# Kernel optimization log

Hardware: AMD Instinct MI355X
Metric: run time of the kernel (lower is better)

## Reference

```python
import jax, jax.numpy as jnp
import numpy as np

B = 131072
SD, AD, HID = 24, 8, 32
NH = SD + AD            # n_heads = 32
UNITS = HID * NH        # 1024


def _xavier(k, shape):
    fan_in, fan_out = shape[-2], shape[-1]
    lim = float(np.sqrt(6.0 / (fan_in + fan_out)))
    return jax.random.uniform(k, shape, jnp.float32, -lim, lim)


def setup_inputs() -> dict:
    key = jax.random.key(0)
    ks = jax.random.split(key, 8)
    return dict(
        state=jax.random.normal(ks[0], (B, SD), jnp.float32),
        action=jax.random.normal(ks[1], (B, AD), jnp.float32),
        # ripple layer 1: per-head Linear(NH -> HID), gate logits init 0 (init_prob=0.5)
        W1=_xavier(ks[2], (NH, NH, HID)), b1=jnp.zeros((NH, HID), jnp.float32), g1=jnp.zeros((NH,), jnp.float32),
        # ripple layer 2: per-head Linear(UNITS -> HID)
        W2=_xavier(ks[3], (NH, UNITS, HID)), b2=jnp.zeros((NH, HID), jnp.float32), g2=jnp.zeros((NH,), jnp.float32),
        # q_network
        Wq1=_xavier(ks[4], (UNITS, 256)), bq1=jnp.zeros((256,), jnp.float32),
        ln1_g=jnp.ones((256,), jnp.float32), ln1_b=jnp.zeros((256,), jnp.float32),
        Wq2=_xavier(ks[5], (256, 128)), bq2=jnp.zeros((128,), jnp.float32),
        ln2_g=jnp.ones((128,), jnp.float32), ln2_b=jnp.zeros((128,), jnp.float32),
        Wq3=_xavier(ks[6], (128, 1)), bq3=jnp.zeros((1,), jnp.float32),
    )


def _ripple(x, W, b, g):
    # x: [B, D]; W: [H, D, K]; per-head linear + tanh, scaled by per-head sigmoid gate
    h = jnp.tanh(jnp.einsum('bd,hdk->bhk', x, W) + b[None])  # [B, H, K]
    h = h * jax.nn.sigmoid(g)[None, :, None]
    return h.reshape(x.shape[0], -1)  # [B, H*K]


def _ln(x, g, b, eps=1e-5):
    mu = jnp.mean(x, -1, keepdims=True)
    var = jnp.mean((x - mu) ** 2, -1, keepdims=True)
    return (x - mu) * jax.lax.rsqrt(var + eps) * g + b


def reference(state, action, W1, b1, g1, W2, b2, g2,
              Wq1, bq1, ln1_g, ln1_b, Wq2, bq2, ln2_g, ln2_b, Wq3, bq3):
    sa = jnp.concatenate([state, action], axis=1)          # [B, SD+AD]
    x = _ripple(sa, W1, b1, g1)                            # [B, UNITS]
    x = _ripple(x, W2, b2, g2)                             # [B, UNITS]
    h = jax.nn.relu(_ln(x @ Wq1 + bq1, ln1_g, ln1_b))      # [B, 256] (dropout = eval identity)
    h = jax.nn.relu(_ln(h @ Wq2 + bq2, ln2_g, ln2_b))      # [B, 128]
    return h @ Wq3 + bq3                                   # [B, 1]
```

## Files before the change

kernel.cpp:

```cpp
#include <hip/hip_runtime.h>
#include <hip/hip_bf16.h>

typedef _Float16 f16x8 __attribute__((ext_vector_type(8)));
typedef float f32x4 __attribute__((ext_vector_type(4)));

__device__ __forceinline__ void async16(const _Float16* g, _Float16* l) {
  __builtin_amdgcn_global_load_lds(
      (const __attribute__((address_space(1))) unsigned int*)g,
      (__attribute__((address_space(3))) unsigned int*)l, 16, 0, 0);
}

__device__ __forceinline__ float tanh_fast(float x) {
  float e = __expf(2.0f * x);
  return 1.0f - 2.0f * __builtin_amdgcn_rcpf(e + 1.0f);
}
__device__ __forceinline__ float sigmoid_fast(float x) {
  return __builtin_amdgcn_rcpf(1.0f + __expf(-x));
}

__global__ __launch_bounds__(256) void transpose_all(
    const float* __restrict__ W1, const float* __restrict__ W2,
    const float* __restrict__ Wq1, const float* __restrict__ Wq2,
    _Float16* __restrict__ V1t, _Float16* __restrict__ V2t,
    _Float16* __restrict__ T1t, _Float16* __restrict__ T2t) {
  __shared__ float tile[32][33];
  int b = blockIdx.x;
  const float* in; _Float16* out; int R, C, rt, ct;
  if (b < 32) {
    in = W1 + b * 1024; out = V1t + b * 1024; R = 32; C = 32; rt = 0; ct = 0;
  } else if (b < 32 + 1024) {
    int i = b - 32; int z = i >> 5;
    in = W2 + (size_t)z * 32768; out = V2t + (size_t)z * 32768;
    R = 1024; C = 32; rt = i & 31; ct = 0;
  } else if (b < 32 + 1024 + 256) {
    int i = b - 1056; in = Wq1; out = T1t; R = 1024; C = 256; rt = i >> 3; ct = i & 7;
  } else {
    int i = b - 1312; in = Wq2; out = T2t; R = 256; C = 128; rt = i >> 2; ct = i & 3;
  }
  int r0 = rt * 32, c0 = ct * 32;
  int t = threadIdx.x;
  int cc = t & 31, rr8 = t >> 5;
#pragma unroll
  for (int p = 0; p < 4; ++p) {
    int r = rr8 + p * 8;
    tile[cc][r] = in[(size_t)(r0 + r) * C + c0 + cc];
  }
  __syncthreads();
  int rr = t & 31, cc8 = t >> 5;
#pragma unroll
  for (int p = 0; p < 4; ++p) {
    int c = cc8 + p * 8;
    out[(size_t)(c0 + c) * R + r0 + rr] = (_Float16)tile[c][rr];
  }
}

__global__ __launch_bounds__(256) void k1_ripple1(
    const float* __restrict__ state, const float* __restrict__ action,
    const _Float16* __restrict__ v1t, const float* __restrict__ b1,
    const float* __restrict__ g1, _Float16* __restrict__ x1, int gro) {
  __shared__ __align__(16) _Float16 As[128 * 40];
  int bn = blockIdx.x, bm = blockIdx.y;
  int t = threadIdx.x, w = t >> 6, l = t & 63, q = l >> 4, l15 = l & 15;
  int n0 = bn * 128, m0 = bm * 128;

  {
    int r = t >> 1, half = t & 1;
    size_t grow = (size_t)(gro + m0 + r);
    float v[16];
    if (half == 0) {
      const float4* sp = (const float4*)(state + grow * 24);
      ((float4*)v)[0] = sp[0]; ((float4*)v)[1] = sp[1];
      ((float4*)v)[2] = sp[2]; ((float4*)v)[3] = sp[3];
    } else {
      const float4* sp = (const float4*)(state + grow * 24 + 16);
      ((float4*)v)[0] = sp[0]; ((float4*)v)[1] = sp[1];
      const float4* ap = (const float4*)(action + grow * 8);
      ((float4*)v)[2] = ap[0]; ((float4*)v)[3] = ap[1];
    }
    f16x8 h0, h1;
#pragma unroll
    for (int j = 0; j < 8; ++j) { h0[j] = (_Float16)v[j]; h1[j] = (_Float16)v[8 + j]; }
    *(f16x8*)&As[r * 40 + half * 16] = h0;
    *(f16x8*)&As[r * 40 + half * 16 + 8] = h1;
  }
  __syncthreads();

  int wr = w >> 1, wc = w & 1;
  f16x8 af[4], bf[4];
#pragma unroll
  for (int mi = 0; mi < 4; ++mi)
    af[mi] = *(const f16x8*)&As[(wr * 64 + mi * 16 + l15) * 40 + q * 8];
#pragma unroll
  for (int ni = 0; ni < 4; ++ni)
    bf[ni] = *(const f16x8*)(v1t + (size_t)(n0 + wc * 64 + ni * 16 + l15) * 32 + q * 8);

  f32x4 acc[4][4] = {};
#pragma unroll
  for (int mi = 0; mi < 4; ++mi)
#pragma unroll
    for (int ni = 0; ni < 4; ++ni)
      acc[mi][ni] = __builtin_amdgcn_mfma_f32_16x16x32_f16(af[mi], bf[ni], acc[mi][ni], 0, 0, 0);

  for (int ni = 0; ni < 4; ++ni) {
    __syncthreads();
    int col = n0 + wc * 64 + ni * 16 + l15;
    float sg = sigmoid_fast(g1[col >> 5]);
    float bias = b1[col];
    int cl = wc * 16 + l15;
#pragma unroll
    for (int mi = 0; mi < 4; ++mi)
#pragma unroll
      for (int r = 0; r < 4; ++r) {
        int rl = wr * 64 + mi * 16 + q * 4 + r;
        As[rl * 40 + cl] = (_Float16)(tanh_fast(acc[mi][ni][r] + bias) * sg);
      }
    __syncthreads();
#pragma unroll
    for (int i = 0; i < 2; ++i) {
      int c = t + i * 256;
      int row = c >> 2, sub = c & 3;
      int colg = n0 + (sub >> 1) * 64 + ni * 16 + (sub & 1) * 8;
      *(float4*)(x1 + (size_t)(m0 + row) * 1024 + colg) = *(const float4*)&As[row * 40 + sub * 8];
    }
  }
}

__global__ __launch_bounds__(256, 4) void k2_ripple2(
    const _Float16* __restrict__ x1, const _Float16* __restrict__ v2t,
    const float* __restrict__ b2, const float* __restrict__ g2,
    _Float16* __restrict__ x2, int nbm) {
  __shared__ __align__(16) _Float16 SMEM[9216];
  _Float16* As = SMEM;
  _Float16* Bs = SMEM + 4096;
  int g = blockIdx.x;
  int bn, bm;
  if ((nbm & 7) == 0) {
    int x = g & 7, j = g >> 3;
    bn = j & 7; bm = x + 8 * (j >> 3);
  } else { bn = g & 7; bm = g >> 3; }
  int t = threadIdx.x, w = t >> 6, l = t & 63, q = l >> 4, l15 = l & 15;
  int n0 = bn * 128, m0 = bm * 128;
  int wr = w >> 1, wc = w & 1;
  f32x4 acc[4][4] = {};

  int c0 = t, c1 = t + 256;
  const _Float16* aS0 = x1 + (size_t)(m0 + (c0 >> 2)) * 1024 + ((c0 & 3) ^ ((c0 >> 3) & 3)) * 8;
  const _Float16* aS1 = x1 + (size_t)(m0 + (c1 >> 2)) * 1024 + ((c1 & 3) ^ ((c1 >> 3) & 3)) * 8;
  const _Float16* bS0 = v2t + (size_t)(n0 + (c0 >> 2)) * 1024 + ((c0 & 3) ^ ((c0 >> 3) & 3)) * 8;
  const _Float16* bS1 = v2t + (size_t)(n0 + (c1 >> 2)) * 1024 + ((c1 & 3) ^ ((c1 >> 3) & 3)) * 8;
  _Float16* aD0 = As + c0 * 8; _Float16* aD1 = As + c1 * 8;
  _Float16* bD0 = Bs + c0 * 8; _Float16* bD1 = Bs + c1 * 8;
  int qs = q ^ ((l15 >> 1) & 3);

  for (int kt = 0; kt < 32; ++kt) {
    __syncthreads();
    int ko = kt * 32;
    async16(aS0 + ko, aD0);
    async16(aS1 + ko, aD1);
    async16(bS0 + ko, bD0);
    async16(bS1 + ko, bD1);
    __builtin_amdgcn_s_waitcnt(0);
    __syncthreads();
    f16x8 af[4], bf[4];
#pragma unroll
    for (int mi = 0; mi < 4; ++mi)
      af[mi] = *(const f16x8*)&As[(wr * 64 + mi * 16 + l15) * 32 + qs * 8];
#pragma unroll
    for (int ni = 0; ni < 4; ++ni)
      bf[ni] = *(const f16x8*)&Bs[(wc * 64 + ni * 16 + l15) * 32 + qs * 8];
#pragma unroll
    for (int mi = 0; mi < 4; ++mi)
#pragma unroll
      for (int ni = 0; ni < 4; ++ni)
        acc[mi][ni] = __builtin_amdgcn_mfma_f32_16x16x32_f16(af[mi], bf[ni], acc[mi][ni], 0, 0, 0);
  }

  for (int pass = 0; pass < 2; ++pass) {
    __syncthreads();
#pragma unroll
    for (int ni2 = 0; ni2 < 2; ++ni2) {
      int ni = pass * 2 + ni2;
      int col = n0 + wc * 64 + ni * 16 + l15;
      float sg = sigmoid_fast(g2[col >> 5]);
      float bias = b2[col];
      int cl = wc * 32 + ni2 * 16 + l15;
#pragma unroll
      for (int mi = 0; mi < 4; ++mi)
#pragma unroll
        for (int r = 0; r < 4; ++r) {
          int rl = wr * 64 + mi * 16 + q * 4 + r;
          SMEM[rl * 72 + cl] = (_Float16)(tanh_fast(acc[mi][ni][r] + bias) * sg);
        }
    }
    __syncthreads();
#pragma unroll
    for (int i = 0; i < 4; ++i) {
      int c = t + i * 256;
      int row = c >> 3, sub = c & 7;
      int colg = n0 + (sub >> 2) * 64 + (pass * 2 + ((sub >> 1) & 1)) * 16 + (sub & 1) * 8;
      *(float4*)(x2 + (size_t)(m0 + row) * 1024 + colg) = *(const float4*)&SMEM[row * 72 + sub * 8];
    }
  }
}

__global__ __launch_bounds__(512, 4) void k3_head(
    const _Float16* __restrict__ x2, const _Float16* __restrict__ t1t,
    const _Float16* __restrict__ t2t,
    const float* __restrict__ bq1, const float* __restrict__ ln1g, const float* __restrict__ ln1b,
    const float* __restrict__ bq2, const float* __restrict__ ln2g, const float* __restrict__ ln2b,
    const float* __restrict__ wq3, const float* __restrict__ bq3,
    float* __restrict__ out) {
  __shared__ __align__(16) _Float16 y1h[128 * 264];
  __shared__ float redA[128 * 4], redB[128 * 4];
  __shared__ float meanv[128], rstdv[128];
  _Float16* Ast = y1h;
  _Float16* Bst = y1h + 4096;
  int bm = blockIdx.x;
  int t = threadIdx.x, w = t >> 6, l = t & 63, q = l >> 4, l15 = l & 15;
  int wr = w >> 2, wc = w & 3;
  int m0 = bm * 128;
  int qs = q ^ ((l15 >> 1) & 3);

  f32x4 acc[4][4] = {};
  const _Float16* aS = x2 + (size_t)(m0 + (t >> 2)) * 1024 + ((t & 3) ^ ((t >> 3) & 3)) * 8;
  _Float16* aD = Ast + t * 8;
  int cb0 = t, cb1 = t + 512;
  const _Float16* bS0 = t1t + (size_t)(cb0 >> 2) * 1024 + ((cb0 & 3) ^ ((cb0 >> 3) & 3)) * 8;
  const _Float16* bS1 = t1t + (size_t)(cb1 >> 2) * 1024 + ((cb1 & 3) ^ ((cb1 >> 3) & 3)) * 8;
  _Float16* bD0 = Bst + cb0 * 8;
  _Float16* bD1 = Bst + cb1 * 8;

  for (int kt = 0; kt < 32; ++kt) {
    __syncthreads();
    int ko = kt * 32;
    async16(aS + ko, aD);
    async16(bS0 + ko, bD0);
    async16(bS1 + ko, bD1);
    __builtin_amdgcn_s_waitcnt(0);
    __syncthreads();
    f16x8 af[4], bf[4];
#pragma unroll
    for (int mi = 0; mi < 4; ++mi)
      af[mi] = *(const f16x8*)&Ast[(wr * 64 + mi * 16 + l15) * 32 + qs * 8];
#pragma unroll
    for (int ni = 0; ni < 4; ++ni)
      bf[ni] = *(const f16x8*)&Bst[(wc * 64 + ni * 16 + l15) * 32 + qs * 8];
#pragma unroll
    for (int mi = 0; mi < 4; ++mi)
#pragma unroll
      for (int ni = 0; ni < 4; ++ni)
        acc[mi][ni] = __builtin_amdgcn_mfma_f32_16x16x32_f16(af[mi], bf[ni], acc[mi][ni], 0, 0, 0);
  }

#pragma unroll
  for (int ni = 0; ni < 4; ++ni) {
    int col = wc * 64 + ni * 16 + l15;
    float b = bq1[col];
#pragma unroll
    for (int mi = 0; mi < 4; ++mi)
#pragma unroll
      for (int r = 0; r < 4; ++r) acc[mi][ni][r] += b;
  }
#pragma unroll
  for (int mi = 0; mi < 4; ++mi)
#pragma unroll
    for (int r = 0; r < 4; ++r) {
      int row = wr * 64 + mi * 16 + q * 4 + r;
      float s = 0.f, sq = 0.f;
#pragma unroll
      for (int ni = 0; ni < 4; ++ni) { float v = acc[mi][ni][r]; s += v; sq += v * v; }
#pragma unroll
      for (int off = 1; off < 16; off <<= 1) { s += __shfl_xor(s, off); sq += __shfl_xor(sq, off); }
      if (l15 == 0) { redA[row * 4 + wc] = s; redB[row * 4 + wc] = sq; }
    }
  __syncthreads();
  if (t < 128) {
    float s  = redA[t * 4] + redA[t * 4 + 1] + redA[t * 4 + 2] + redA[t * 4 + 3];
    float sq = redB[t * 4] + redB[t * 4 + 1] + redB[t * 4 + 2] + redB[t * 4 + 3];
    float mean = s * (1.0f / 256.0f);
    float var = sq * (1.0f / 256.0f) - mean * mean;
    meanv[t] = mean; rstdv[t] = rsqrtf(var + 1e-5f);
  }
  __syncthreads();
#pragma unroll
  for (int mi = 0; mi < 4; ++mi)
#pragma unroll
    for (int ni = 0; ni < 4; ++ni)
#pragma unroll
      for (int r = 0; r < 4; ++r) {
        int row = wr * 64 + mi * 16 + q * 4 + r;
        int col = wc * 64 + ni * 16 + l15;
        float y = (acc[mi][ni][r] - meanv[row]) * rstdv[row] * ln1g[col] + ln1b[col];
        y = fmaxf(y, 0.f);
        y1h[row * 264 + col] = (_Float16)y;
      }
  __syncthreads();

  f32x4 a2[4][2] = {};
  for (int kt = 0; kt < 8; ++kt) {
    f16x8 af2[4];
#pragma unroll
    for (int mi = 0; mi < 4; ++mi)
      af2[mi] = *(const f16x8*)&y1h[(wr * 64 + mi * 16 + l15) * 264 + kt * 32 + q * 8];
#pragma unroll
    for (int ni = 0; ni < 2; ++ni) {
      f16x8 bf = *(const f16x8*)(t2t + (size_t)(wc * 32 + ni * 16 + l15) * 256 + kt * 32 + q * 8);
#pragma unroll
      for (int mi = 0; mi < 4; ++mi)
        a2[mi][ni] = __builtin_amdgcn_mfma_f32_16x16x32_f16(af2[mi], bf, a2[mi][ni], 0, 0, 0);
    }
  }
#pragma unroll
  for (int ni = 0; ni < 2; ++ni) {
    int col = wc * 32 + ni * 16 + l15;
    float b = bq2[col];
#pragma unroll
    for (int mi = 0; mi < 4; ++mi)
#pragma unroll
      for (int r = 0; r < 4; ++r) a2[mi][ni][r] += b;
  }
  __syncthreads();
#pragma unroll
  for (int mi = 0; mi < 4; ++mi)
#pragma unroll
    for (int r = 0; r < 4; ++r) {
      int row = wr * 64 + mi * 16 + q * 4 + r;
      float s = 0.f, sq = 0.f;
#pragma unroll
      for (int ni = 0; ni < 2; ++ni) { float v = a2[mi][ni][r]; s += v; sq += v * v; }
#pragma unroll
      for (int off = 1; off < 16; off <<= 1) { s += __shfl_xor(s, off); sq += __shfl_xor(sq, off); }
      if (l15 == 0) { redA[row * 4 + wc] = s; redB[row * 4 + wc] = sq; }
    }
  __syncthreads();
  if (t < 128) {
    float s  = redA[t * 4] + redA[t * 4 + 1] + redA[t * 4 + 2] + redA[t * 4 + 3];
    float sq = redB[t * 4] + redB[t * 4 + 1] + redB[t * 4 + 2] + redB[t * 4 + 3];
    float mean = s * (1.0f / 128.0f);
    float var = sq * (1.0f / 128.0f) - mean * mean;
    meanv[t] = mean; rstdv[t] = rsqrtf(var + 1e-5f);
  }
  __syncthreads();
#pragma unroll
  for (int mi = 0; mi < 4; ++mi)
#pragma unroll
    for (int r = 0; r < 4; ++r) {
      int row = wr * 64 + mi * 16 + q * 4 + r;
      float pr = 0.f;
#pragma unroll
      for (int ni = 0; ni < 2; ++ni) {
        int col = wc * 32 + ni * 16 + l15;
        float y = (a2[mi][ni][r] - meanv[row]) * rstdv[row] * ln2g[col] + ln2b[col];
        y = fmaxf(y, 0.f);
        pr += y * wq3[col];
      }
#pragma unroll
      for (int off = 1; off < 16; off <<= 1) pr += __shfl_xor(pr, off);
      if (l15 == 0) redA[row * 4 + wc] = pr;
    }
  __syncthreads();
  if (t < 128)
    out[m0 + t] = redA[t * 4] + redA[t * 4 + 1] + redA[t * 4 + 2] + redA[t * 4 + 3] + bq3[0];
}

extern "C" void kernel_launch(void* const* d_in, const int* in_sizes, int n_in,
                              void* d_out, int out_size, void* d_ws, size_t ws_size,
                              hipStream_t stream) {
  const float* state  = (const float*)d_in[0];
  const float* action = (const float*)d_in[1];
  const float* W1  = (const float*)d_in[2];
  const float* b1  = (const float*)d_in[3];
  const float* g1  = (const float*)d_in[4];
  const float* W2  = (const float*)d_in[5];
  const float* b2  = (const float*)d_in[6];
  const float* g2  = (const float*)d_in[7];
  const float* Wq1 = (const float*)d_in[8];
  const float* bq1 = (const float*)d_in[9];
  const float* ln1g = (const float*)d_in[10];
  const float* ln1b = (const float*)d_in[11];
  const float* Wq2 = (const float*)d_in[12];
  const float* bq2 = (const float*)d_in[13];
  const float* ln2g = (const float*)d_in[14];
  const float* ln2b = (const float*)d_in[15];
  const float* Wq3 = (const float*)d_in[16];
  const float* bq3 = (const float*)d_in[17];
  int B = in_sizes[0] / 24;

  char* ws = (char*)d_ws;
  _Float16* V1t = (_Float16*)(ws);
  _Float16* V2t = (_Float16*)(ws + 65536);
  _Float16* T1t = (_Float16*)(ws + 65536 + 2097152);
  _Float16* T2t = (_Float16*)(ws + 65536 + 2097152 + 524288);
  size_t woff = (65536 + 2097152 + 524288 + 65536 + 4095) & ~(size_t)4095;

  size_t avail = ws_size > woff ? ws_size - woff : 0;
  int S, G;
  if (avail >= (size_t)32768 * 2048 * 3) {
    S = 32768; G = 2;
  } else {
    long rows = (long)(avail / 4096);
    if (rows > 32768) rows = 32768;
    rows &= ~127L;
    if (rows < 128) rows = 128;
    S = (int)rows; G = 1;
  }
  _Float16* x1 = (_Float16*)(ws + woff);
  _Float16* x2 = x1 + (size_t)S * 1024;

  transpose_all<<<1344, 256, 0, stream>>>(W1, W2, Wq1, Wq2, V1t, V2t, T1t, T2t);

  int nsl = (B + S - 1) / S;
  for (int i = 0; i < nsl; ++i) {
    int r0 = i * S;
    int Sc = S < (B - r0) ? S : (B - r0);
    int nbm = Sc / 128;
    k1_ripple1<<<dim3(8, nbm), 256, 0, stream>>>(state, action, V1t, b1, g1, x1, r0);
    k2_ripple2<<<dim3(8 * nbm), 256, 0, stream>>>(x1, V2t, b2, g2,
                                                  x2 + (size_t)(i % G) * S * 1024, nbm);
    if (i % G == G - 1 || i == nsl - 1) {
      int gstart = (i - i % G) * S;
      int nrows = r0 + Sc - gstart;
      k3_head<<<dim3(nrows / 128), 512, 0, stream>>>(x2, T1t, T2t, bq1, ln1g, ln1b,
                                                     bq2, ln2g, ln2b, Wq3, bq3,
                                                     (float*)d_out + gstart);
    }
  }
}
```

Baseline: 694.4 us.

## Register-prefetch A tiles with double-buffered LDS and load weight fragments directly

In the ripple-2 and head GEMM kernels, the A tile is now prefetched into registers one k-step ahead and written into a double-buffered LDS region. This replaces the async global-to-LDS copy that was followed by a full waitcnt and two barriers. The B (weight) fragments are now loaded straight from global memory into registers, skipping LDS, on the expectation that the small weight matrices stay cache-resident. The aim is to overlap global latency with MFMA work and to reduce barriers and LDS traffic, at the cost of higher register pressure (k2 occupancy hint drops from 4 to 3) and uncoalesced per-lane global loads for B.

```diff
diff --git a/kernel.cpp b/kernel.cpp
--- a/kernel.cpp
+++ b/kernel.cpp
@@ -3,12 +3,6 @@
 
 typedef _Float16 f16x8 __attribute__((ext_vector_type(8)));
 typedef float f32x4 __attribute__((ext_vector_type(4)));
-
-__device__ __forceinline__ void async16(const _Float16* g, _Float16* l) {
-  __builtin_amdgcn_global_load_lds(
-      (const __attribute__((address_space(1))) unsigned int*)g,
-      (__attribute__((address_space(3))) unsigned int*)l, 16, 0, 0);
-}
 
 __device__ __forceinline__ float tanh_fast(float x) {
   float e = __expf(2.0f * x);
@@ -125,13 +119,11 @@
   }
 }
 
-__global__ __launch_bounds__(256, 4) void k2_ripple2(
+__global__ __launch_bounds__(256, 3) void k2_ripple2(
     const _Float16* __restrict__ x1, const _Float16* __restrict__ v2t,
     const float* __restrict__ b2, const float* __restrict__ g2,
     _Float16* __restrict__ x2, int nbm) {
   __shared__ __align__(16) _Float16 SMEM[9216];
-  _Float16* As = SMEM;
-  _Float16* Bs = SMEM + 4096;
   int g = blockIdx.x;
   int bn, bm;
   if ((nbm & 7) == 0) {
@@ -146,28 +138,32 @@
   int c0 = t, c1 = t + 256;
   const _Float16* aS0 = x1 + (size_t)(m0 + (c0 >> 2)) * 1024 + ((c0 & 3) ^ ((c0 >> 3) & 3)) * 8;
   const _Float16* aS1 = x1 + (size_t)(m0 + (c1 >> 2)) * 1024 + ((c1 & 3) ^ ((c1 >> 3) & 3)) * 8;
-  const _Float16* bS0 = v2t + (size_t)(n0 + (c0 >> 2)) * 1024 + ((c0 & 3) ^ ((c0 >> 3) & 3)) * 8;
-  const _Float16* bS1 = v2t + (size_t)(n0 + (c1 >> 2)) * 1024 + ((c1 & 3) ^ ((c1 >> 3) & 3)) * 8;
-  _Float16* aD0 = As + c0 * 8; _Float16* aD1 = As + c1 * 8;
-  _Float16* bD0 = Bs + c0 * 8; _Float16* bD1 = Bs + c1 * 8;
+  const _Float16* bP[4];
+#pragma unroll
+  for (int ni = 0; ni < 4; ++ni)
+    bP[ni] = v2t + (size_t)(n0 + wc * 64 + ni * 16 + l15) * 1024 + q * 8;
   int qs = q ^ ((l15 >> 1) & 3);
 
+  f16x8 ra0 = *(const f16x8*)aS0;
+  f16x8 ra1 = *(const f16x8*)aS1;
+
   for (int kt = 0; kt < 32; ++kt) {
-    __syncthreads();
-    int ko = kt * 32;
-    async16(aS0 + ko, aD0);
-    async16(aS1 + ko, aD1);
-    async16(bS0 + ko, bD0);
-    async16(bS1 + ko, bD1);
-    __builtin_amdgcn_s_waitcnt(0);
-    __syncthreads();
-    f16x8 af[4], bf[4];
-#pragma unroll
-    for (int mi = 0; mi < 4; ++mi)
-      af[mi] = *(const f16x8*)&As[(wr * 64 + mi * 16 + l15) * 32 + qs * 8];
+    _Float16* buf = SMEM + (kt & 1) * 4096;
+    *(f16x8*)(buf + c0 * 8) = ra0;
+    *(f16x8*)(buf + c1 * 8) = ra1;
+    __syncthreads();
+    if (kt < 31) {
+      ra0 = *(const f16x8*)(aS0 + (kt + 1) * 32);
+      ra1 = *(const f16x8*)(aS1 + (kt + 1) * 32);
+    }
+    f16x8 bf[4];
 #pragma unroll
     for (int ni = 0; ni < 4; ++ni)
-      bf[ni] = *(const f16x8*)&Bs[(wc * 64 + ni * 16 + l15) * 32 + qs * 8];
+      bf[ni] = *(const f16x8*)(bP[ni] + kt * 32);
+    f16x8 af[4];
+#pragma unroll
+    for (int mi = 0; mi < 4; ++mi)
+      af[mi] = *(const f16x8*)&buf[(wr * 64 + mi * 16 + l15) * 32 + qs * 8];
 #pragma unroll
     for (int mi = 0; mi < 4; ++mi)
 #pragma unroll
@@ -213,8 +209,6 @@
   __shared__ __align__(16) _Float16 y1h[128 * 264];
   __shared__ float redA[128 * 4], redB[128 * 4];
   __shared__ float meanv[128], rstdv[128];
-  _Float16* Ast = y1h;
-  _Float16* Bst = y1h + 4096;
   int bm = blockIdx.x;
   int t = threadIdx.x, w = t >> 6, l = t & 63, q = l >> 4, l15 = l & 15;
   int wr = w >> 2, wc = w & 3;
@@ -223,33 +217,32 @@
 
   f32x4 acc[4][4] = {};
   const _Float16* aS = x2 + (size_t)(m0 + (t >> 2)) * 1024 + ((t & 3) ^ ((t >> 3) & 3)) * 8;
-  _Float16* aD = Ast + t * 8;
-  int cb0 = t, cb1 = t + 512;
-  const _Float16* bS0 = t1t + (size_t)(cb0 >> 2) * 1024 + ((cb0 & 3) ^ ((cb0 >> 3) & 3)) * 8;
-  const _Float16* bS1 = t1t + (size_t)(cb1 >> 2) * 1024 + ((cb1 & 3) ^ ((cb1 >> 3) & 3)) * 8;
-  _Float16* bD0 = Bst + cb0 * 8;
-  _Float16* bD1 = Bst + cb1 * 8;
+  const _Float16* bP[4];
+#pragma unroll
+  for (int ni = 0; ni < 4; ++ni)
+    bP[ni] = t1t + (size_t)(wc * 64 + ni * 16 + l15) * 1024 + q * 8;
+
+  f16x8 ra = *(const f16x8*)aS;
 
   for (int kt = 0; kt < 32; ++kt) {
-    __syncthreads();
-    int ko = kt * 32;
-    async16(aS + ko, aD);
-    async16(bS0 + ko, bD0);
-    async16(bS1 + ko, bD1);
-    __builtin_amdgcn_s_waitcnt(0);
-    __syncthreads();
-    f16x8 af[4], bf[4];
-#pragma unroll
-    for (int mi = 0; mi < 4; ++mi)
-      af[mi] = *(const f16x8*)&Ast[(wr * 64 + mi * 16 + l15) * 32 + qs * 8];
+    _Float16* buf = y1h + (kt & 1) * 4096;
+    *(f16x8*)(buf + t * 8) = ra;
+    __syncthreads();
+    if (kt < 31) ra = *(const f16x8*)(aS + (kt + 1) * 32);
+    f16x8 bf[4];
 #pragma unroll
     for (int ni = 0; ni < 4; ++ni)
-      bf[ni] = *(const f16x8*)&Bst[(wc * 64 + ni * 16 + l15) * 32 + qs * 8];
+      bf[ni] = *(const f16x8*)(bP[ni] + kt * 32);
+    f16x8 af[4];
+#pragma unroll
+    for (int mi = 0; mi < 4; ++mi)
+      af[mi] = *(const f16x8*)&buf[(wr * 64 + mi * 16 + l15) * 32 + qs * 8];
 #pragma unroll
     for (int mi = 0; mi < 4; ++mi)
 #pragma unroll
       for (int ni = 0; ni < 4; ++ni)
         acc[mi][ni] = __builtin_amdgcn_mfma_f32_16x16x32_f16(af[mi], bf[ni], acc[mi][ni], 0, 0, 0);
+    __syncthreads();
   }
 
 #pragma unroll
```

Measured after the change: 970.3 us. 39.7% more time.
